# Kernel tuning notes

Measured on AMD Instinct MI355X. Metric: run time of the kernel, lower is better.

Reference implementation:

```python
import jax, jax.numpy as jnp
import numpy as np

B, S, D, H = 4, 2048, 1024, 16
HD = D // H

def setup_inputs() -> dict:
    key = jax.random.key(0)
    k1, k2, k3, k4, k5 = jax.random.split(key, 5)
    sc = 1.0 / np.sqrt(D)
    return {
        "x": jax.random.normal(k1, (B, S, D), dtype=jnp.float32),
        "w_qkv": jax.random.normal(k2, (D, 3 * D), dtype=jnp.float32) * sc,
        "b_qkv": jnp.zeros((3 * D,), dtype=jnp.float32),
        "w_proj": jax.random.normal(k3, (D, D), dtype=jnp.float32) * sc,
        "b_proj": jnp.zeros((D,), dtype=jnp.float32),
    }

def reference(x, w_qkv, b_qkv, w_proj, b_proj):
    bsz, seq_len, dim = x.shape
    qkv = x @ w_qkv + b_qkv                      # [B,S,3D]
    q, k, v = jnp.split(qkv, 3, axis=2)
    q = q.reshape(bsz, seq_len, H, HD).transpose(0, 2, 1, 3)  # [B,H,S,hd]
    k = k.reshape(bsz, seq_len, H, HD).transpose(0, 2, 1, 3)
    v = v.reshape(bsz, seq_len, H, HD).transpose(0, 2, 1, 3)
    att = jnp.einsum('bhqd,bhkd->bhqk', q, k) * (1.0 / np.sqrt(HD))
    causal = jnp.tril(jnp.ones((seq_len, seq_len), dtype=bool))
    att = jnp.where(causal[None, None], att, -jnp.inf)
    att = jax.nn.softmax(att, axis=-1)
    y = jnp.einsum('bhqk,bhkd->bhqd', att, v)
    y = y.transpose(0, 2, 1, 3).reshape(bsz, seq_len, dim)
    return y @ w_proj + b_proj
```

## Files before the change

### kernel.cpp

```cpp
#include <hip/hip_runtime.h>
#include <cstdint>
#include <cstddef>

typedef float  f32x4  __attribute__((ext_vector_type(4)));
typedef __bf16 bf16x8 __attribute__((ext_vector_type(8)));
typedef __bf16 bf16x4 __attribute__((ext_vector_type(4)));

#define DEVI static __device__ __forceinline__

DEVI f32x4 mfma_bf16(bf16x8 a, bf16x8 b, f32x4 c) {
  return __builtin_amdgcn_mfma_f32_16x16x32_bf16(a, b, c, 0, 0, 0);
}

DEVI void gload_lds16(const void* g, void* l) {
  __builtin_amdgcn_global_load_lds(
      (const __attribute__((address_space(1))) void*)g,
      (__attribute__((address_space(3))) void*)l, 16, 0, 0);
}

__global__ __launch_bounds__(256) void k_prep(
    const float* __restrict__ x, __bf16* __restrict__ xb,
    const float* __restrict__ w_qkv, __bf16* __restrict__ wqkvT,
    const float* __restrict__ w_proj, __bf16* __restrict__ wprojT) {
  __shared__ __bf16 tile[64][65];
  const int idx = blockIdx.x;
  if (idx < 8192) {
    int i = idx * 256 + threadIdx.x;
    float4 v = reinterpret_cast<const float4*>(x)[i];
    bf16x4 r;
    r.x = (__bf16)v.x; r.y = (__bf16)v.y; r.z = (__bf16)v.z; r.w = (__bf16)v.w;
    reinterpret_cast<bf16x4*>(xb)[i] = r;
    return;
  }
  const float* src; __bf16* dst; int R, C, bx, by;
  if (idx < 8960) {
    int id2 = idx - 8192; bx = id2 % 48; by = id2 / 48;
    src = w_qkv; dst = wqkvT; R = 1024; C = 3072;
  } else {
    int id2 = idx - 8960; bx = id2 % 16; by = id2 / 16;
    src = w_proj; dst = wprojT; R = 1024; C = 1024;
  }
  const int tx = threadIdx.x & 63, ty = threadIdx.x >> 6;
  const int r0 = by * 64, c0 = bx * 64;
#pragma unroll
  for (int i = 0; i < 16; ++i) {
    int r = ty * 16 + i;
    tile[r][tx] = (__bf16)src[(size_t)(r0 + r) * C + c0 + tx];
  }
  __syncthreads();
#pragma unroll
  for (int i = 0; i < 16; ++i) {
    int c = ty * 16 + i;
    dst[(size_t)(c0 + c) * R + r0 + tx] = tile[tx][c];
  }
}

template <int MODE>
__global__ __launch_bounds__(256, 2) void k_gemm_bt(
    const __bf16* __restrict__ A, const __bf16* __restrict__ Bt,
    const float* __restrict__ bias, void* __restrict__ Cv,
    __bf16* __restrict__ VT,
    int M, int N, int K, int nbx) {
  __shared__ __bf16 As[128 * 64];
  __shared__ __bf16 Bs[128 * 64];
  const int t = threadIdx.x;
  const int w = t >> 6, lane = t & 63;
  const int l15 = lane & 15, lg = lane >> 4;
  const int nwg = gridDim.x;
  const int wgid = (blockIdx.x & 7) * (nwg >> 3) + (blockIdx.x >> 3);
  const int m0 = (wgid / nbx) * 128;
  const int n0 = (wgid % nbx) * 128;
  const int wr = w >> 1, wc = w & 1;
  const int lrow = lane >> 3, lslot = lane & 7;

  f32x4 acc[4][4] = {};

  const int nK = K >> 6;
  for (int kt = 0; kt < nK; ++kt) {
    const __bf16* Ab = A + (size_t)m0 * K + kt * 64;
    const __bf16* Bb = Bt + (size_t)n0 * K + kt * 64;
#pragma unroll
    for (int c = 0; c < 4; ++c) {
      int seg = w * 4 + c;
      int row = seg * 8 + lrow;
      int cb = (lslot ^ (row & 7)) << 4;
      gload_lds16((const char*)(Ab + (size_t)row * K) + cb, (char*)As + seg * 1024);
      gload_lds16((const char*)(Bb + (size_t)row * K) + cb, (char*)Bs + seg * 1024);
    }
    __syncthreads();
#pragma unroll
    for (int ks = 0; ks < 2; ++ks) {
      bf16x8 af[4], bfr[4];
      const int cb = ks * 64 + (lg << 4);
#pragma unroll
      for (int m = 0; m < 4; ++m) {
        int row = wr * 64 + m * 16 + l15;
        af[m] = *(const bf16x8*)((const char*)As + row * 128 + (cb ^ ((row & 7) << 4)));
      }
#pragma unroll
      for (int n = 0; n < 4; ++n) {
        int row = wc * 64 + n * 16 + l15;
        bfr[n] = *(const bf16x8*)((const char*)Bs + row * 128 + (cb ^ ((row & 7) << 4)));
      }
#pragma unroll
      for (int m = 0; m < 4; ++m)
#pragma unroll
        for (int n = 0; n < 4; ++n)
          acc[m][n] = mfma_bf16(af[m], bfr[n], acc[m][n]);
    }
    __syncthreads();
  }

  const bool vsec = (MODE == 0) && (VT != nullptr) && (n0 >= 2048);
#pragma unroll
  for (int n = 0; n < 4; ++n) {
    const int gcol = n0 + wc * 64 + n * 16 + l15;
    const float bv = bias ? bias[gcol] : 0.0f;
#pragma unroll
    for (int m = 0; m < 4; ++m) {
      const int grow = m0 + wr * 64 + m * 16 + (lg << 2);
      if (vsec) {
        const int hd = gcol - 2048;
        const int b = grow >> 11, s0v = grow & 2047;
        const int nib = (s0v >> 2) & 15;
        const int nib2 = (nib < 4) ? 2 * nib : (nib < 8) ? 2 * nib - 7
                        : (nib < 12) ? 2 * nib - 8 : 2 * nib - 15;
        const int sp = (s0v & ~63) | (nib2 << 2);
        bf16x4 pkv;
#pragma unroll
        for (int r = 0; r < 4; ++r) pkv[r] = (__bf16)(acc[m][n][r] + bv);
        *(bf16x4*)(VT + ((size_t)(b * 16) * 64 + hd) * 2048 + sp) = pkv;
      } else {
#pragma unroll
        for (int r = 0; r < 4; ++r) {
          float v = acc[m][n][r] + bv;
          if (MODE == 0)
            ((__bf16*)Cv)[(size_t)(grow + r) * N + gcol] = (__bf16)v;
          else
            ((float*)Cv)[(size_t)(grow + r) * N + gcol] = v;
        }
      }
    }
  }
}

__global__ __launch_bounds__(512, 2) void k_attn(
    const __bf16* __restrict__ qkv,
    const __bf16* __restrict__ VT,
    __bf16* __restrict__ Y) {
  __shared__ __bf16 kbuf[2][64 * 64];
  __shared__ __bf16 vbuf[2][64 * 64];
  const int t = threadIdx.x, w = t >> 6, lane = t & 63;
  const int l15 = lane & 15, lg = lane >> 4;
  const int bid = blockIdx.x;
  const int g = bid >> 6;
  const int qt = (g < 4) ? 15 - g : (g < 8) ? g - 4 : (g < 12) ? 19 - g : g - 8;
  const int bh = bid & 63;
  const int b = bh >> 4, h = bh & 15;
  const int q0 = qt * 128;
  const int nkv = 2 * qt + 2;
  const float SCL = 0.125f * 1.44269504f;

  const size_t qrow = (size_t)(b * 2048 + q0 + w * 16 + l15);
  const bf16x8 qf0 = *(const bf16x8*)(qkv + qrow * 3072 + h * 64 + lg * 8);
  const bf16x8 qf1 = *(const bf16x8*)(qkv + qrow * 3072 + h * 64 + 32 + lg * 8);

  const __bf16* kg = qkv + (size_t)(b * 2048) * 3072 + 1024 + h * 64;
  const __bf16* vg = VT + (size_t)bh * 64 * 2048;

  const int srow = t >> 3, sslot = t & 7;
  const int sb = (sslot ^ (srow & 7)) << 4;
  auto stage = [&](int bi, int kvi) {
    gload_lds16((const char*)(kg + (size_t)(kvi * 64 + srow) * 3072) + sb,
                (char*)kbuf[bi] + w * 1024);
    gload_lds16((const char*)(vg + (size_t)srow * 2048 + kvi * 64) + sb,
                (char*)vbuf[bi] + w * 1024);
  };

  f32x4 o[4] = {};
  float mr = -1e30f, lr = 0.0f;

  stage(0, 0);
  asm volatile("s_waitcnt vmcnt(0)" ::: "memory");
  __syncthreads();

  for (int kv = 0; kv < nkv; ++kv) {
    if (kv + 1 < nkv) stage((kv + 1) & 1, kv + 1);
    const char* kb = (const char*)kbuf[kv & 1];
    const char* vb = (const char*)vbuf[kv & 1];

    f32x4 s[4] = {};
    __builtin_amdgcn_s_setprio(1);
#pragma unroll
    for (int nb = 0; nb < 4; ++nb) {
      int row = nb * 16 + l15;
      int sw = (row & 7) << 4;
      bf16x8 k0 = *(const bf16x8*)(kb + row * 128 + ((lg * 16) ^ sw));
      bf16x8 k1 = *(const bf16x8*)(kb + row * 128 + ((64 + lg * 16) ^ sw));
      s[nb] = mfma_bf16(k0, qf0, s[nb]);
      s[nb] = mfma_bf16(k1, qf1, s[nb]);
    }
    __builtin_amdgcn_s_setprio(0);

    if (((kv + 1) << 6) > q0 + w * 16) {
      const int qg = q0 + w * 16 + l15;
#pragma unroll
      for (int nb = 0; nb < 4; ++nb)
#pragma unroll
        for (int r = 0; r < 4; ++r)
          if (kv * 64 + nb * 16 + lg * 4 + r > qg) s[nb][r] = -1e30f;
    }

    float a0 = fmaxf(fmaxf(s[0][0], s[0][1]), s[0][2]);
    float a1 = fmaxf(fmaxf(s[0][3], s[1][0]), s[1][1]);
    float a2 = fmaxf(fmaxf(s[1][2], s[1][3]), s[2][0]);
    float a3 = fmaxf(fmaxf(s[2][1], s[2][2]), s[2][3]);
    float a4 = fmaxf(fmaxf(s[3][0], s[3][1]), s[3][2]);
    float pm = fmaxf(fmaxf(fmaxf(a0, a1), a2), fmaxf(fmaxf(a3, a4), s[3][3]));
    pm = fmaxf(pm, __shfl_xor(pm, 16));
    pm = fmaxf(pm, __shfl_xor(pm, 32));
    pm *= SCL;

    if (!__all(pm <= mr + 8.0f)) {
      float nm = fmaxf(mr, pm);
      float alpha = __builtin_amdgcn_exp2f(mr - nm);
      lr *= alpha;
      mr = nm;
#pragma unroll
      for (int r = 0; r < 4; ++r) {
        float aO = __shfl(alpha, lg * 4 + r);
        o[0][r] *= aO; o[1][r] *= aO; o[2][r] *= aO; o[3][r] *= aO;
      }
    }

    float psum = 0.0f;
    bf16x4 pk[4];
#pragma unroll
    for (int nb = 0; nb < 4; ++nb) {
      f32x4 pe;
#pragma unroll
      for (int r = 0; r < 4; ++r)
        pe[r] = __builtin_amdgcn_exp2f(fmaf(s[nb][r], SCL, -mr));
      psum += (pe[0] + pe[1]) + (pe[2] + pe[3]);
      pk[nb][0] = (__bf16)pe[0]; pk[nb][1] = (__bf16)pe[1];
      pk[nb][2] = (__bf16)pe[2]; pk[nb][3] = (__bf16)pe[3];
    }
    psum += __shfl_xor(psum, 16);
    psum += __shfl_xor(psum, 32);
    lr += psum;

    const bf16x8 pf0 = __builtin_shufflevector(pk[0], pk[1], 0, 1, 2, 3, 4, 5, 6, 7);
    const bf16x8 pf1 = __builtin_shufflevector(pk[2], pk[3], 0, 1, 2, 3, 4, 5, 6, 7);
    __builtin_amdgcn_s_setprio(1);
#pragma unroll
    for (int nb = 0; nb < 4; ++nb) {
      int row = nb * 16 + l15;
      int sw = (row & 7) << 4;
      bf16x8 v0 = *(const bf16x8*)(vb + row * 128 + ((lg * 16) ^ sw));
      bf16x8 v1 = *(const bf16x8*)(vb + row * 128 + ((64 + lg * 16) ^ sw));
      o[nb] = mfma_bf16(pf0, v0, o[nb]);
      o[nb] = mfma_bf16(pf1, v1, o[nb]);
    }
    __builtin_amdgcn_s_setprio(0);
    asm volatile("s_waitcnt vmcnt(0)" ::: "memory");
    __syncthreads();
  }

  float lO[4];
#pragma unroll
  for (int r = 0; r < 4; ++r) lO[r] = __shfl(lr, lg * 4 + r);
#pragma unroll
  for (int nb = 0; nb < 4; ++nb)
#pragma unroll
    for (int r = 0; r < 4; ++r) {
      float v = o[nb][r] / lO[r];
      size_t row = (size_t)(b * 2048 + q0 + w * 16 + lg * 4 + r);
      Y[row * 1024 + h * 64 + nb * 16 + l15] = (__bf16)v;
    }
}

extern "C" void kernel_launch(void* const* d_in, const int* in_sizes, int n_in,
                              void* d_out, int out_size, void* d_ws, size_t ws_size,
                              hipStream_t stream) {
  const float* x      = (const float*)d_in[0];
  const float* w_qkv  = (const float*)d_in[1];
  const float* b_qkv  = (const float*)d_in[2];
  const float* w_proj = (const float*)d_in[3];
  const float* b_proj = (const float*)d_in[4];
  float* out = (float*)d_out;

  char* ws = (char*)d_ws;
  const size_t MB = 1024 * 1024;
  __bf16* xb     = (__bf16*)(ws);
  __bf16* wqkvT  = (__bf16*)(ws + 16 * MB);
  __bf16* wprojT = (__bf16*)(ws + 22 * MB);
  __bf16* qkv    = (__bf16*)(ws + 24 * MB);
  __bf16* VT     = (__bf16*)(ws + 72 * MB);
  __bf16* Y      = (__bf16*)(ws + 88 * MB);

  k_prep<<<dim3(9216), 256, 0, stream>>>(x, xb, w_qkv, wqkvT, w_proj, wprojT);
  k_gemm_bt<0><<<dim3(64 * 24), 256, 0, stream>>>(xb, wqkvT, b_qkv, qkv, VT, 8192, 3072, 1024, 24);
  k_attn<<<dim3(1024), 512, 0, stream>>>(qkv, VT, Y);
  k_gemm_bt<1><<<dim3(64 * 8), 256, 0, stream>>>(Y, wprojT, b_proj, out, nullptr, 8192, 1024, 1024, 8);
}
```

Baseline: 166.9 us.

## Split heavy causal query tiles across two KV halves and merge partials

The eight heaviest query tiles (qt>=8) are each split into two work items covering separate halves of the KV range. Each half writes its unnormalized partial output along with its running max and sum, and a new merge kernel combines the two halves into Y. The order in which query tiles are scheduled is now packed into lookup constants to balance load across the larger grid. The GEMM's XCD-aware block remapping is also removed, which is a separate scheduling change. The split adds an extra launch and extra partial traffic, and the partial outputs are stored in bf16 before merging, which may cost some accuracy.

```diff
diff --git a/kernel.cpp b/kernel.cpp
--- a/kernel.cpp
+++ b/kernel.cpp
@@ -66,10 +66,8 @@
   const int t = threadIdx.x;
   const int w = t >> 6, lane = t & 63;
   const int l15 = lane & 15, lg = lane >> 4;
-  const int nwg = gridDim.x;
-  const int wgid = (blockIdx.x & 7) * (nwg >> 3) + (blockIdx.x >> 3);
-  const int m0 = (wgid / nbx) * 128;
-  const int n0 = (wgid % nbx) * 128;
+  const int m0 = (blockIdx.x / nbx) * 128;
+  const int n0 = (blockIdx.x % nbx) * 128;
   const int wr = w >> 1, wc = w & 1;
   const int lrow = lane >> 3, lslot = lane & 7;
 
@@ -147,18 +145,24 @@
 __global__ __launch_bounds__(512, 2) void k_attn(
     const __bf16* __restrict__ qkv,
     const __bf16* __restrict__ VT,
-    __bf16* __restrict__ Y) {
+    __bf16* __restrict__ Y,
+    __bf16* __restrict__ Opart,
+    float* __restrict__ ML) {
   __shared__ __bf16 kbuf[2][64 * 64];
   __shared__ __bf16 vbuf[2][64 * 64];
   const int t = threadIdx.x, w = t >> 6, lane = t & 63;
   const int l15 = lane & 15, lg = lane >> 4;
   const int bid = blockIdx.x;
-  const int g = bid >> 6;
-  const int qt = (g < 4) ? 15 - g : (g < 8) ? g - 4 : (g < 12) ? 19 - g : g - 8;
+  const int o = bid >> 6;
   const int bh = bid & 63;
   const int b = bh >> 4, h = bh & 15;
-  const int q0 = qt * 128;
-  const int nkv = 2 * qt + 2;
+  const int qt = (o < 16) ? (int)((0x9AA5BBCC6DDEE7FFull >> (o * 4)) & 15ull)
+                          : (int)((0x01238849u >> ((o - 16) * 4)) & 15u);
+  const int heavy = (0xDEF7B >> o) & 1;
+  const int halfsel = heavy ? ((0x94A52 >> o) & 1) : -1;
+  const int q0 = qt << 7;
+  const int kv0 = (halfsel == 1) ? qt + 1 : 0;
+  const int kv1 = (halfsel == 0) ? qt + 1 : 2 * qt + 2;
   const float SCL = 0.125f * 1.44269504f;
 
   const size_t qrow = (size_t)(b * 2048 + q0 + w * 16 + l15);
@@ -177,15 +181,15 @@
                 (char*)vbuf[bi] + w * 1024);
   };
 
-  f32x4 o[4] = {};
+  f32x4 o4[4] = {};
   float mr = -1e30f, lr = 0.0f;
 
-  stage(0, 0);
+  stage(kv0 & 1, kv0);
   asm volatile("s_waitcnt vmcnt(0)" ::: "memory");
   __syncthreads();
 
-  for (int kv = 0; kv < nkv; ++kv) {
-    if (kv + 1 < nkv) stage((kv + 1) & 1, kv + 1);
+  for (int kv = kv0; kv < kv1; ++kv) {
+    if (kv + 1 < kv1) stage((kv + 1) & 1, kv + 1);
     const char* kb = (const char*)kbuf[kv & 1];
     const char* vb = (const char*)vbuf[kv & 1];
 
@@ -229,7 +233,7 @@
 #pragma unroll
       for (int r = 0; r < 4; ++r) {
         float aO = __shfl(alpha, lg * 4 + r);
-        o[0][r] *= aO; o[1][r] *= aO; o[2][r] *= aO; o[3][r] *= aO;
+        o4[0][r] *= aO; o4[1][r] *= aO; o4[2][r] *= aO; o4[3][r] *= aO;
       }
     }
 
@@ -258,25 +262,69 @@
       int sw = (row & 7) << 4;
       bf16x8 v0 = *(const bf16x8*)(vb + row * 128 + ((lg * 16) ^ sw));
       bf16x8 v1 = *(const bf16x8*)(vb + row * 128 + ((64 + lg * 16) ^ sw));
-      o[nb] = mfma_bf16(pf0, v0, o[nb]);
-      o[nb] = mfma_bf16(pf1, v1, o[nb]);
+      o4[nb] = mfma_bf16(pf0, v0, o4[nb]);
+      o4[nb] = mfma_bf16(pf1, v1, o4[nb]);
     }
     __builtin_amdgcn_s_setprio(0);
     asm volatile("s_waitcnt vmcnt(0)" ::: "memory");
     __syncthreads();
   }
 
-  float lO[4];
-#pragma unroll
-  for (int r = 0; r < 4; ++r) lO[r] = __shfl(lr, lg * 4 + r);
-#pragma unroll
-  for (int nb = 0; nb < 4; ++nb)
-#pragma unroll
-    for (int r = 0; r < 4; ++r) {
-      float v = o[nb][r] / lO[r];
-      size_t row = (size_t)(b * 2048 + q0 + w * 16 + lg * 4 + r);
-      Y[row * 1024 + h * 64 + nb * 16 + l15] = (__bf16)v;
-    }
+  if (halfsel < 0) {
+    float lO[4];
+#pragma unroll
+    for (int r = 0; r < 4; ++r) lO[r] = __shfl(lr, lg * 4 + r);
+#pragma unroll
+    for (int nb = 0; nb < 4; ++nb)
+#pragma unroll
+      for (int r = 0; r < 4; ++r) {
+        float v = o4[nb][r] / lO[r];
+        size_t row = (size_t)(b * 2048 + q0 + w * 16 + lg * 4 + r);
+        Y[row * 1024 + h * 64 + nb * 16 + l15] = (__bf16)v;
+      }
+  } else {
+    const int pid = bh * 8 + (qt - 8);
+    __bf16* op = Opart + (size_t)(pid * 2 + halfsel) * 8192;
+#pragma unroll
+    for (int nb = 0; nb < 4; ++nb)
+#pragma unroll
+      for (int r = 0; r < 4; ++r)
+        op[(w * 16 + lg * 4 + r) * 64 + nb * 16 + l15] = (__bf16)o4[nb][r];
+    if (lg == 0) {
+      float2 ml; ml.x = mr; ml.y = lr;
+      ((float2*)ML)[(pid * 2 + halfsel) * 128 + w * 16 + l15] = ml;
+    }
+  }
+}
+
+__global__ __launch_bounds__(256) void k_merge(
+    const __bf16* __restrict__ Opart, const float* __restrict__ ML,
+    __bf16* __restrict__ Y) {
+  const int bid = blockIdx.x;
+  const int bh = bid & 63, j = bid >> 6;
+  const int pid = bh * 8 + j;
+  const int qt = 8 + j, b = bh >> 4, h = bh & 15;
+  const int t = threadIdx.x;
+  const int row = t >> 1, ch = t & 1;
+  const __bf16* oa = Opart + (size_t)(pid * 2 + 0) * 8192 + row * 64 + ch * 32;
+  const __bf16* ob = Opart + (size_t)(pid * 2 + 1) * 8192 + row * 64 + ch * 32;
+  const float2 mlA = ((const float2*)ML)[(pid * 2 + 0) * 128 + row];
+  const float2 mlB = ((const float2*)ML)[(pid * 2 + 1) * 128 + row];
+  const float m = fmaxf(mlA.x, mlB.x);
+  const float eA = __builtin_amdgcn_exp2f(mlA.x - m);
+  const float eB = __builtin_amdgcn_exp2f(mlB.x - m);
+  const float rl = 1.0f / (eA * mlA.y + eB * mlB.y);
+  __bf16* yp = Y + (size_t)(b * 2048 + (qt << 7) + row) * 1024 + h * 64 + ch * 32;
+#pragma unroll
+  for (int i = 0; i < 4; ++i) {
+    bf16x8 av = ((const bf16x8*)oa)[i];
+    bf16x8 bv = ((const bf16x8*)ob)[i];
+    bf16x8 res;
+#pragma unroll
+    for (int k = 0; k < 8; ++k)
+      res[k] = (__bf16)((eA * (float)av[k] + eB * (float)bv[k]) * rl);
+    ((bf16x8*)yp)[i] = res;
+  }
 }
 
 extern "C" void kernel_launch(void* const* d_in, const int* in_sizes, int n_in,
@@ -297,9 +345,12 @@
   __bf16* qkv    = (__bf16*)(ws + 24 * MB);
   __bf16* VT     = (__bf16*)(ws + 72 * MB);
   __bf16* Y      = (__bf16*)(ws + 88 * MB);
+  __bf16* Opart  = (__bf16*)(ws);
+  float*  ML     = (float*)(ws + 16 * MB);
 
   k_prep<<<dim3(9216), 256, 0, stream>>>(x, xb, w_qkv, wqkvT, w_proj, wprojT);
   k_gemm_bt<0><<<dim3(64 * 24), 256, 0, stream>>>(xb, wqkvT, b_qkv, qkv, VT, 8192, 3072, 1024, 24);
-  k_attn<<<dim3(1024), 512, 0, stream>>>(qkv, VT, Y);
+  k_attn<<<dim3(1536), 512, 0, stream>>>(qkv, VT, Y, Opart, ML);
+  k_merge<<<dim3(512), 256, 0, stream>>>(Opart, ML, Y);
   k_gemm_bt<1><<<dim3(64 * 8), 256, 0, stream>>>(Y, wprojT, b_proj, out, nullptr, 8192, 1024, 1024, 8);
 }
```

Result: slower. 172.5 us (+3.4%).
